# Performance work log

Hardware: AMD Instinct MI355X
Metric: run time of the kernel (lower is better)

The kernel has to match this reference:

```python
import jax, jax.numpy as jnp
import numpy as np

B, L, D_MODEL = 2, 2048, 1024
N_HEADS, D_K = 16, 64  # d_v == d_k (required by the output*q epilogue)


def setup_inputs() -> dict:
    key = jax.random.key(0)
    ks = jax.random.split(key, 8)
    # xavier_normal std for [d_model, d_k] fan: sqrt(2/(d_model+d_k))
    std = float(np.sqrt(2.0 / (D_MODEL + D_K)))
    std_p = float(np.sqrt(1.0 / (N_HEADS * D_K)))  # nn.Linear default ~ U(-1/sqrt(fan_in),..); normal approx ok for a baseline
    return {
        "q": jax.random.normal(ks[0], (B, L, D_MODEL), jnp.float32),
        "k": jax.random.normal(ks[1], (B, L, D_MODEL), jnp.float32),
        "v": jax.random.normal(ks[2], (B, L, D_MODEL), jnp.float32),
        "w_qs": jax.random.normal(ks[3], (N_HEADS, D_MODEL, D_K), jnp.float32) * std,
        "w_ks": jax.random.normal(ks[4], (N_HEADS, D_MODEL, D_K), jnp.float32) * std,
        "w_vs": jax.random.normal(ks[5], (N_HEADS, D_MODEL, D_K), jnp.float32) * std,
        "w_proj": jax.random.normal(ks[6], (D_MODEL, N_HEADS * D_K), jnp.float32) * std_p,
        "b_proj": jnp.zeros((D_MODEL,), jnp.float32),
    }


def reference(q, k, v, w_qs, w_ks, w_vs, w_proj, b_proj):
    # Per-head projections: [h, B, L, d_k]
    qh = jnp.einsum("bld,hdk->hblk", q, w_qs)
    kh = jnp.einsum("bld,hdk->hblk", k, w_ks)
    vh = jnp.einsum("bld,hdk->hblk", v, w_vs)
    # UNscaled attention (no 1/sqrt(d_k)), dropout is identity at eval
    attn = jax.nn.softmax(jnp.einsum("hblk,hbmk->hblm", qh, kh), axis=-1)
    # attn @ V with elementwise *q epilogue
    out = jnp.einsum("hblm,hbmk->hblk", attn, vh) * qh
    # torch.cat(torch.split(outputs, mb_size, 0), -1): heads concat on last dim
    out = out.transpose(1, 2, 0, 3).reshape(q.shape[0], q.shape[1], -1)  # [B, L, h*d_k]
    return out @ w_proj.T + b_proj
```

## Files before the change

kernel.cpp:

```cpp
#include <hip/hip_runtime.h>

#define B_ 2
#define L_ 2048
#define DM 1024
#define H_ 16
#define DK 64
#define ROWS (B_*L_)
#define BK 32
#define LDT 40

typedef _Float16 f16x8 __attribute__((ext_vector_type(8)));
typedef float    f32x4 __attribute__((ext_vector_type(4)));
typedef unsigned short us8 __attribute__((ext_vector_type(8)));
typedef unsigned short us4v __attribute__((ext_vector_type(4)));

__device__ __forceinline__ unsigned short f2h(float f) {
    _Float16 h = (_Float16)f;
    return __builtin_bit_cast(unsigned short, h);
}
__device__ __forceinline__ float h2f(unsigned short u) {
    return (float)__builtin_bit_cast(_Float16, u);
}
__device__ __forceinline__ f16x8 ld8h(const unsigned short* p) {
    return *reinterpret_cast<const f16x8*>(p);
}
__device__ __forceinline__ us8 cvt_us8(float4 a, float4 b) {
    us8 u;
    u[0] = f2h(a.x); u[1] = f2h(a.y); u[2] = f2h(a.z); u[3] = f2h(a.w);
    u[4] = f2h(b.x); u[5] = f2h(b.y); u[6] = f2h(b.z); u[7] = f2h(b.w);
    return u;
}

#define MFMA(a, b, c) __builtin_amdgcn_mfma_f32_16x16x32_f16((a), (b), (c), 0, 0, 0)

__global__ __launch_bounds__(256) void kcvt(
    const float* __restrict__ src, unsigned short* __restrict__ dst)
{
    size_t i = ((size_t)blockIdx.x * 256 + threadIdx.x) * 8;
    const float4* s4 = (const float4*)(src + i);
    *(us8*)(dst + i) = cvt_us8(s4[0], s4[1]);
}

__global__ __launch_bounds__(256) void k0_transpose_w(
    const float* __restrict__ wq,
    const float* __restrict__ wk,
    const float* __restrict__ wv,
    unsigned short* __restrict__ wt)
{
    __shared__ unsigned short tile[64][65];
    int bx = blockIdx.x;
    int which = bx / (H_ * 16);
    int rem   = bx % (H_ * 16);
    int h  = rem >> 4;
    int db = (rem & 15) * 64;
    const float* src = (which == 0) ? wq : (which == 1) ? wk : wv;

    int t = threadIdx.x;
    int r = t >> 2;
    int c = (t & 3) * 16;
    const float4* sp = (const float4*)(src + ((size_t)(h * DM + db + r)) * DK + c);
    #pragma unroll
    for (int i4 = 0; i4 < 4; i4++) {
        float4 f = sp[i4];
        tile[r][c + i4 * 4 + 0] = f2h(f.x);
        tile[r][c + i4 * 4 + 1] = f2h(f.y);
        tile[r][c + i4 * 4 + 2] = f2h(f.z);
        tile[r][c + i4 * 4 + 3] = f2h(f.w);
    }
    __syncthreads();

    int n   = t >> 2;
    int d16 = (t & 3) * 16;
    __align__(16) unsigned short ov[16];
    #pragma unroll
    for (int i = 0; i < 16; i++) ov[i] = tile[d16 + i][n];
    size_t off = (((size_t)which * H_ + h) * DK + n) * DM + db + d16;
    *(us8*)(wt + off)     = *(us8*)&ov[0];
    *(us8*)(wt + off + 8) = *(us8*)&ov[8];
}

__global__ __launch_bounds__(256) void k1_proj_qkv(
    const float* __restrict__ q,
    const float* __restrict__ k,
    const float* __restrict__ v,
    const unsigned short* __restrict__ wt,
    unsigned short* __restrict__ qh,
    unsigned short* __restrict__ kh,
    unsigned short* __restrict__ vt)
{
    __shared__ __align__(16) unsigned short sA[128 * LDT];
    __shared__ __align__(16) unsigned short sB[128 * LDT];

    int bx = blockIdx.x;
    int which = bx >> 8;
    int rem   = bx & 255;
    int mbase = (rem >> 3) * 128;
    int nbase = (rem & 7) * 128;

    const float* Ag = (which == 0) ? q : (which == 1) ? k : v;
    const unsigned short* Bg = wt + (size_t)which * DM * DM;

    int t = threadIdx.x;
    int wave = t >> 6, lane = t & 63, quad = lane >> 4, l16 = lane & 15;
    int wm = (wave >> 1) * 64, wn = (wave & 1) * 64;

    int ar0 = t >> 2,         ac0 = t & 3;
    int ar1 = (256 + t) >> 2, ac1 = t & 3;
    const float* pA0 = Ag + (size_t)(mbase + ar0) * DM + ac0 * 8;
    const float* pA1 = Ag + (size_t)(mbase + ar1) * DM + ac1 * 8;
    const unsigned short* pB0 = Bg + (size_t)(nbase + ar0) * DM + ac0 * 8;
    const unsigned short* pB1 = Bg + (size_t)(nbase + ar1) * DM + ac1 * 8;
    unsigned short* wA0 = &sA[ar0 * LDT + ac0 * 8];
    unsigned short* wA1 = &sA[ar1 * LDT + ac1 * 8];
    unsigned short* wB0 = &sB[ar0 * LDT + ac0 * 8];
    unsigned short* wB1 = &sB[ar1 * LDT + ac1 * 8];

    f32x4 acc[4][4];
    #pragma unroll
    for (int mi = 0; mi < 4; mi++)
        #pragma unroll
        for (int ni = 0; ni < 4; ni++) acc[mi][ni] = (f32x4)0.0f;

    float4 rA0a = *(const float4*)pA0, rA0b = *(const float4*)(pA0 + 4);
    float4 rA1a = *(const float4*)pA1, rA1b = *(const float4*)(pA1 + 4);
    us8 rB0 = *(const us8*)pB0, rB1 = *(const us8*)pB1;

    for (int step = 0; step < 32; step++) {
        if (step) __syncthreads();
        *(us8*)wA0 = cvt_us8(rA0a, rA0b);
        *(us8*)wA1 = cvt_us8(rA1a, rA1b);
        *(us8*)wB0 = rB0; *(us8*)wB1 = rB1;
        __syncthreads();
        if (step < 31) {
            pA0 += BK; pA1 += BK; pB0 += BK; pB1 += BK;
            rA0a = *(const float4*)pA0; rA0b = *(const float4*)(pA0 + 4);
            rA1a = *(const float4*)pA1; rA1b = *(const float4*)(pA1 + 4);
            rB0 = *(const us8*)pB0; rB1 = *(const us8*)pB1;
        }
        f16x8 aF[4], bF[4];
        #pragma unroll
        for (int mi = 0; mi < 4; mi++)
            aF[mi] = *(const f16x8*)&sA[(wm + mi * 16 + l16) * LDT + quad * 8];
        #pragma unroll
        for (int ni = 0; ni < 4; ni++)
            bF[ni] = *(const f16x8*)&sB[(wn + ni * 16 + l16) * LDT + quad * 8];
        #pragma unroll
        for (int mi = 0; mi < 4; mi++)
            #pragma unroll
            for (int ni = 0; ni < 4; ni++)
                acc[mi][ni] = MFMA(aF[mi], bF[ni], acc[mi][ni]);
    }

    int h = (nbase >> 6) + (wave & 1);
    if (which < 2) {
        unsigned short* OUT = ((which == 0) ? qh : kh) + (size_t)h * ROWS * DK;
        #pragma unroll
        for (int mi = 0; mi < 4; mi++)
            #pragma unroll
            for (int ni = 0; ni < 4; ni++)
                #pragma unroll
                for (int r = 0; r < 4; r++) {
                    int row = mbase + wm + mi * 16 + quad * 4 + r;
                    OUT[(size_t)row * DK + ni * 16 + l16] = f2h(acc[mi][ni][r]);
                }
    } else {
        unsigned short* OUT = vt + (size_t)h * DK * ROWS;
        #pragma unroll
        for (int mi = 0; mi < 4; mi++)
            #pragma unroll
            for (int ni = 0; ni < 4; ni++) {
                int dk   = ni * 16 + l16;
                int rowb = mbase + wm + mi * 16 + quad * 4;
                us4v pk;
                pk[0] = f2h(acc[mi][ni][0]); pk[1] = f2h(acc[mi][ni][1]);
                pk[2] = f2h(acc[mi][ni][2]); pk[3] = f2h(acc[mi][ni][3]);
                *(us4v*)(OUT + (size_t)dk * ROWS + rowb) = pk;
            }
    }
}

__global__ __launch_bounds__(256) void k2_attn(
    const unsigned short* __restrict__ qh,
    const unsigned short* __restrict__ kh,
    const unsigned short* __restrict__ vt,
    unsigned short* __restrict__ x2)
{
    __shared__ __align__(16) unsigned short ktile[64][72];
    __shared__ __align__(16) unsigned short vtile[64][72];
    __shared__ __align__(16) unsigned short pld[4][16][72];

    int bx = blockIdx.x;
    int xcd = bx & 7;
    int loc = bx >> 3;
    int hb  = xcd * 4 + (loc >> 5);
    int qt  = loc & 31;
    int h = hb >> 1, b = hb & 1;
    int qbase = qt * 64;

    const unsigned short* qhp = qh + ((size_t)h * ROWS + b * L_) * DK;
    const unsigned short* khp = kh + ((size_t)h * ROWS + b * L_) * DK;
    const unsigned short* vtp = vt + (size_t)h * DK * ROWS + b * L_;

    int wave = threadIdx.x >> 6, lane = threadIdx.x & 63;
    int quad = lane >> 4, l16 = lane & 15;
    int t = threadIdx.x;

    int qrow = qbase + wave * 16 + l16;
    f16x8 qb0 = ld8h(qhp + (size_t)qrow * DK + quad * 8);
    f16x8 qb1 = ld8h(qhp + (size_t)qrow * DK + 32 + quad * 8);

    float m_i = -1e30f, l_i = 0.0f;
    f32x4 o[4];
    #pragma unroll
    for (int nt = 0; nt < 4; nt++) o[nt] = (f32x4)0.0f;

    for (int kt = 0; kt < 32; kt++) {
        int kb = kt * 64;
        {
            const unsigned short* kg = khp + (size_t)kb * DK;
            #pragma unroll
            for (int i = 0; i < 2; i++) {
                int c = i * 256 + t;
                int key = c >> 3, ch = (c & 7) * 8;
                *(us8*)&ktile[key][ch] = *(const us8*)(kg + c * 8);
            }
            #pragma unroll
            for (int i = 0; i < 2; i++) {
                int c = i * 256 + t;
                int dk = c >> 3, ch = (c & 7) * 8;
                *(us8*)&vtile[dk][ch] = *(const us8*)(vtp + (size_t)dk * ROWS + kb + ch);
            }
        }
        __syncthreads();

        f32x4 s[4];
        #pragma unroll
        for (int nt = 0; nt < 4; nt++) s[nt] = (f32x4)0.0f;
        #pragma unroll
        for (int nt = 0; nt < 4; nt++) {
            f16x8 ka0 = *(const f16x8*)&ktile[nt * 16 + l16][quad * 8];
            f16x8 ka1 = *(const f16x8*)&ktile[nt * 16 + l16][32 + quad * 8];
            s[nt] = MFMA(ka0, qb0, s[nt]);
            s[nt] = MFMA(ka1, qb1, s[nt]);
        }

        float mx = s[0][0];
        #pragma unroll
        for (int nt = 0; nt < 4; nt++)
            #pragma unroll
            for (int r = 0; r < 4; r++) mx = fmaxf(mx, s[nt][r]);
        mx = fmaxf(mx, __shfl_xor(mx, 16));
        mx = fmaxf(mx, __shfl_xor(mx, 32));
        float mnew  = fmaxf(m_i, mx);
        float alpha = __expf(m_i - mnew);
        float rs = 0.0f;
        #pragma unroll
        for (int nt = 0; nt < 4; nt++)
            #pragma unroll
            for (int r = 0; r < 4; r++) {
                float pv = __expf(s[nt][r] - mnew);
                s[nt][r] = pv;
                rs += pv;
            }
        rs += __shfl_xor(rs, 16);
        rs += __shfl_xor(rs, 32);
        l_i = l_i * alpha + rs;
        m_i = mnew;

        #pragma unroll
        for (int r = 0; r < 4; r++) {
            float av = __shfl(alpha, quad * 4 + r);
            #pragma unroll
            for (int nt = 0; nt < 4; nt++) o[nt][r] *= av;
        }

        #pragma unroll
        for (int nt = 0; nt < 4; nt++) {
            us4v pk;
            pk[0] = f2h(s[nt][0]); pk[1] = f2h(s[nt][1]);
            pk[2] = f2h(s[nt][2]); pk[3] = f2h(s[nt][3]);
            *(us4v*)&pld[wave][l16][nt * 16 + quad * 4] = pk;
        }

        #pragma unroll
        for (int kk = 0; kk < 2; kk++) {
            f16x8 pa = *(const f16x8*)&pld[wave][l16][kk * 32 + quad * 8];
            #pragma unroll
            for (int nt = 0; nt < 4; nt++) {
                f16x8 vb = *(const f16x8*)&vtile[nt * 16 + l16][kk * 32 + quad * 8];
                o[nt] = MFMA(pa, vb, o[nt]);
            }
        }
        __syncthreads();
    }

    float linv = 1.0f / l_i;
    #pragma unroll
    for (int r = 0; r < 4; r++) {
        float lv = __shfl(linv, quad * 4 + r);
        int row = qbase + wave * 16 + quad * 4 + r;
        #pragma unroll
        for (int nt = 0; nt < 4; nt++) {
            int col = nt * 16 + l16;
            float qv = h2f(qhp[(size_t)row * DK + col]);
            float val = o[nt][r] * lv * qv;
            x2[((size_t)b * L_ + row) * DM + h * DK + col] = f2h(val);
        }
    }
}

__global__ __launch_bounds__(256) void k3_out_proj(
    const unsigned short* __restrict__ x2,
    const unsigned short* __restrict__ wph,
    const float* __restrict__ bias,
    float* __restrict__ out)
{
    __shared__ __align__(16) unsigned short sA[128 * LDT];
    __shared__ __align__(16) unsigned short sB[128 * LDT];

    int bx = blockIdx.x;
    int mbase = (bx >> 3) * 128;
    int nbase = (bx & 7) * 128;

    int t = threadIdx.x;
    int wave = t >> 6, lane = t & 63, quad = lane >> 4, l16 = lane & 15;
    int wm = (wave >> 1) * 64, wn = (wave & 1) * 64;

    int ar0 = t >> 2,         ac0 = t & 3;
    int ar1 = (256 + t) >> 2, ac1 = t & 3;
    const unsigned short* pA0 = x2 + (size_t)(mbase + ar0) * DM + ac0 * 8;
    const unsigned short* pA1 = x2 + (size_t)(mbase + ar1) * DM + ac1 * 8;
    const unsigned short* pB0 = wph + (size_t)(nbase + ar0) * DM + ac0 * 8;
    const unsigned short* pB1 = wph + (size_t)(nbase + ar1) * DM + ac1 * 8;
    unsigned short* wA0 = &sA[ar0 * LDT + ac0 * 8];
    unsigned short* wA1 = &sA[ar1 * LDT + ac1 * 8];
    unsigned short* wB0 = &sB[ar0 * LDT + ac0 * 8];
    unsigned short* wB1 = &sB[ar1 * LDT + ac1 * 8];

    f32x4 acc[4][4];
    #pragma unroll
    for (int mi = 0; mi < 4; mi++)
        #pragma unroll
        for (int ni = 0; ni < 4; ni++) acc[mi][ni] = (f32x4)0.0f;

    us8 rA0 = *(const us8*)pA0, rA1 = *(const us8*)pA1;
    us8 rB0 = *(const us8*)pB0, rB1 = *(const us8*)pB1;

    for (int step = 0; step < 32; step++) {
        if (step) __syncthreads();
        *(us8*)wA0 = rA0; *(us8*)wA1 = rA1;
        *(us8*)wB0 = rB0; *(us8*)wB1 = rB1;
        __syncthreads();
        if (step < 31) {
            pA0 += BK; pA1 += BK; pB0 += BK; pB1 += BK;
            rA0 = *(const us8*)pA0; rA1 = *(const us8*)pA1;
            rB0 = *(const us8*)pB0; rB1 = *(const us8*)pB1;
        }
        f16x8 aF[4], bF[4];
        #pragma unroll
        for (int mi = 0; mi < 4; mi++)
            aF[mi] = *(const f16x8*)&sA[(wm + mi * 16 + l16) * LDT + quad * 8];
        #pragma unroll
        for (int ni = 0; ni < 4; ni++)
            bF[ni] = *(const f16x8*)&sB[(wn + ni * 16 + l16) * LDT + quad * 8];
        #pragma unroll
        for (int mi = 0; mi < 4; mi++)
            #pragma unroll
            for (int ni = 0; ni < 4; ni++)
                acc[mi][ni] = MFMA(aF[mi], bF[ni], acc[mi][ni]);
    }

    float bv[4];
    #pragma unroll
    for (int ni = 0; ni < 4; ni++) bv[ni] = bias[nbase + wn + ni * 16 + l16];

    #pragma unroll
    for (int mi = 0; mi < 4; mi++)
        #pragma unroll
        for (int ni = 0; ni < 4; ni++)
            #pragma unroll
            for (int r = 0; r < 4; r++) {
                int row = mbase + wm + mi * 16 + quad * 4 + r;
                int col = nbase + wn + ni * 16 + l16;
                out[(size_t)row * DM + col] = acc[mi][ni][r] + bv[ni];
            }
}

extern "C" void kernel_launch(void* const* d_in, const int* in_sizes, int n_in,
                              void* d_out, int out_size, void* d_ws, size_t ws_size,
                              hipStream_t stream)
{
    const float* q     = (const float*)d_in[0];
    const float* k     = (const float*)d_in[1];
    const float* v     = (const float*)d_in[2];
    const float* wqs   = (const float*)d_in[3];
    const float* wks   = (const float*)d_in[4];
    const float* wvs   = (const float*)d_in[5];
    const float* wproj = (const float*)d_in[6];
    const float* bproj = (const float*)d_in[7];
    float* out = (float*)d_out;

    char* ws = (char*)d_ws;
    #define MB (size_t)(1024 * 1024)
    unsigned short* wt  = (unsigned short*)(ws);
    unsigned short* wph = (unsigned short*)(ws + 6  * MB);
    unsigned short* qh  = (unsigned short*)(ws + 8  * MB);
    unsigned short* kh  = (unsigned short*)(ws + 16 * MB);
    unsigned short* vt  = (unsigned short*)(ws + 24 * MB);
    unsigned short* x2  = (unsigned short*)(ws + 32 * MB);

    kcvt<<<dim3((DM * DM) / (256 * 8)), dim3(256), 0, stream>>>(wproj, wph);
    k0_transpose_w<<<dim3(3 * H_ * 16), dim3(256), 0, stream>>>(wqs, wks, wvs, wt);

    k1_proj_qkv<<<dim3(3 * 32 * 8), dim3(256), 0, stream>>>(q, k, v, wt, qh, kh, vt);
    k2_attn<<<dim3(H_ * B_ * 32), dim3(256), 0, stream>>>(qh, kh, vt, x2);
    k3_out_proj<<<dim3(32 * 8), dim3(256), 0, stream>>>(x2, wph, bproj, out);
}
```

Baseline: 263.1 us.

## Double-buffer K tiles, load V directly into registers, lazily rescale softmax

The attention kernel now double-buffers the K tile in shared memory. The next tile is prefetched into registers during compute, so each iteration needs only one barrier instead of two. V fragments are read straight from global memory into registers, skipping the shared-memory V tile. The online softmax only rescales the running max and accumulators when the new row max grows by more than 8, which saves exp and multiply work. The trade-offs are more register pressure, uncoalesced direct global V loads, and a bounded growth of exponent values under the lazy rescale.

```diff
diff --git a/kernel.cpp b/kernel.cpp
--- a/kernel.cpp
+++ b/kernel.cpp
@@ -185,8 +185,7 @@
     const unsigned short* __restrict__ vt,
     unsigned short* __restrict__ x2)
 {
-    __shared__ __align__(16) unsigned short ktile[64][72];
-    __shared__ __align__(16) unsigned short vtile[64][72];
+    __shared__ __align__(16) unsigned short ktile[2][64][72];
     __shared__ __align__(16) unsigned short pld[4][16][72];
 
     int bx = blockIdx.x;
@@ -205,6 +204,9 @@
     int quad = lane >> 4, l16 = lane & 15;
     int t = threadIdx.x;
 
+    int key0 = t >> 3,         kch0 = (t & 7) * 8;
+    int key1 = (256 + t) >> 3, kch1 = (t & 7) * 8;
+
     int qrow = qbase + wave * 16 + l16;
     f16x8 qb0 = ld8h(qhp + (size_t)qrow * DK + quad * 8);
     f16x8 qb1 = ld8h(qhp + (size_t)qrow * DK + 32 + quad * 8);
@@ -214,35 +216,39 @@
     #pragma unroll
     for (int nt = 0; nt < 4; nt++) o[nt] = (f32x4)0.0f;
 
+    us8 kr0 = *(const us8*)(khp + (size_t)t * 8);
+    us8 kr1 = *(const us8*)(khp + (size_t)(256 + t) * 8);
+    *(us8*)&ktile[0][key0][kch0] = kr0;
+    *(us8*)&ktile[0][key1][kch1] = kr1;
+    __syncthreads();
+
+    int cur = 0;
     for (int kt = 0; kt < 32; kt++) {
         int kb = kt * 64;
-        {
-            const unsigned short* kg = khp + (size_t)kb * DK;
-            #pragma unroll
-            for (int i = 0; i < 2; i++) {
-                int c = i * 256 + t;
-                int key = c >> 3, ch = (c & 7) * 8;
-                *(us8*)&ktile[key][ch] = *(const us8*)(kg + c * 8);
-            }
-            #pragma unroll
-            for (int i = 0; i < 2; i++) {
-                int c = i * 256 + t;
-                int dk = c >> 3, ch = (c & 7) * 8;
-                *(us8*)&vtile[dk][ch] = *(const us8*)(vtp + (size_t)dk * ROWS + kb + ch);
-            }
-        }
-        __syncthreads();
 
         f32x4 s[4];
         #pragma unroll
         for (int nt = 0; nt < 4; nt++) s[nt] = (f32x4)0.0f;
         #pragma unroll
         for (int nt = 0; nt < 4; nt++) {
-            f16x8 ka0 = *(const f16x8*)&ktile[nt * 16 + l16][quad * 8];
-            f16x8 ka1 = *(const f16x8*)&ktile[nt * 16 + l16][32 + quad * 8];
+            f16x8 ka0 = *(const f16x8*)&ktile[cur][nt * 16 + l16][quad * 8];
+            f16x8 ka1 = *(const f16x8*)&ktile[cur][nt * 16 + l16][32 + quad * 8];
             s[nt] = MFMA(ka0, qb0, s[nt]);
             s[nt] = MFMA(ka1, qb1, s[nt]);
         }
+
+        if (kt < 31) {
+            const unsigned short* kg = khp + (size_t)(kb + 64) * DK;
+            kr0 = *(const us8*)(kg + (size_t)t * 8);
+            kr1 = *(const us8*)(kg + (size_t)(256 + t) * 8);
+        }
+        f16x8 vbr[2][4];
+        #pragma unroll
+        for (int kk = 0; kk < 2; kk++)
+            #pragma unroll
+            for (int nt = 0; nt < 4; nt++)
+                vbr[kk][nt] = ld8h(vtp + (size_t)(nt * 16 + l16) * ROWS
+                                       + kb + kk * 32 + quad * 8);
 
         float mx = s[0][0];
         #pragma unroll
@@ -251,28 +257,32 @@
             for (int r = 0; r < 4; r++) mx = fmaxf(mx, s[nt][r]);
         mx = fmaxf(mx, __shfl_xor(mx, 16));
         mx = fmaxf(mx, __shfl_xor(mx, 32));
-        float mnew  = fmaxf(m_i, mx);
-        float alpha = __expf(m_i - mnew);
+
+        if (!__all(mx - m_i <= 8.0f)) {
+            float mnew  = fmaxf(m_i, mx);
+            float alpha = __expf(m_i - mnew);
+            l_i *= alpha;
+            #pragma unroll
+            for (int r = 0; r < 4; r++) {
+                float av = __shfl(alpha, quad * 4 + r);
+                #pragma unroll
+                for (int nt = 0; nt < 4; nt++) o[nt][r] *= av;
+            }
+            m_i = mnew;
+        }
+
         float rs = 0.0f;
         #pragma unroll
         for (int nt = 0; nt < 4; nt++)
             #pragma unroll
             for (int r = 0; r < 4; r++) {
-                float pv = __expf(s[nt][r] - mnew);
+                float pv = __expf(s[nt][r] - m_i);
                 s[nt][r] = pv;
                 rs += pv;
             }
         rs += __shfl_xor(rs, 16);
         rs += __shfl_xor(rs, 32);
-        l_i = l_i * alpha + rs;
-        m_i = mnew;
-
-        #pragma unroll
-        for (int r = 0; r < 4; r++) {
-            float av = __shfl(alpha, quad * 4 + r);
-            #pragma unroll
-            for (int nt = 0; nt < 4; nt++) o[nt][r] *= av;
-        }
+        l_i += rs;
 
         #pragma unroll
         for (int nt = 0; nt < 4; nt++) {
@@ -286,12 +296,16 @@
         for (int kk = 0; kk < 2; kk++) {
             f16x8 pa = *(const f16x8*)&pld[wave][l16][kk * 32 + quad * 8];
             #pragma unroll
-            for (int nt = 0; nt < 4; nt++) {
-                f16x8 vb = *(const f16x8*)&vtile[nt * 16 + l16][kk * 32 + quad * 8];
-                o[nt] = MFMA(pa, vb, o[nt]);
-            }
+            for (int nt = 0; nt < 4; nt++)
+                o[nt] = MFMA(pa, vbr[kk][nt], o[nt]);
+        }
+
+        if (kt < 31) {
+            *(us8*)&ktile[cur ^ 1][key0][kch0] = kr0;
+            *(us8*)&ktile[cur ^ 1][key1][kch1] = kr1;
         }
         __syncthreads();
+        cur ^= 1;
     }
 
     float linv = 1.0f / l_i;
```

Result: slower. 338.2 us (+28.5%).

## Use base-2 softmax with log2e folded into K weights and lazy rescaling

Applied to the files above, without the earlier changes.

Multiplies the K projection weights by log2(e) during weight conversion, so attention scores come out in the base-2 domain and the softmax can call the hardware exp2 directly. The running max and the rescaling of the output accumulator are now skipped unless some lane's max grows by more than 11, which saves exps, shuffles and multiplies in most iterations. The max and sum reductions become trees, and s_setprio raises wave priority around the MFMA blocks. In exchange, unnormalized probabilities can reach 2^11, which narrows the fp16 headroom for P, and K is rounded to fp16 after scaling.

```diff
diff --git a/kernel.cpp b/kernel.cpp
--- a/kernel.cpp
+++ b/kernel.cpp
@@ -54,6 +54,7 @@
     int h  = rem >> 4;
     int db = (rem & 15) * 64;
     const float* src = (which == 0) ? wq : (which == 1) ? wk : wv;
+    float scale = (which == 1) ? 1.44269504f : 1.0f;
 
     int t = threadIdx.x;
     int r = t >> 2;
@@ -62,10 +63,10 @@
     #pragma unroll
     for (int i4 = 0; i4 < 4; i4++) {
         float4 f = sp[i4];
-        tile[r][c + i4 * 4 + 0] = f2h(f.x);
-        tile[r][c + i4 * 4 + 1] = f2h(f.y);
-        tile[r][c + i4 * 4 + 2] = f2h(f.z);
-        tile[r][c + i4 * 4 + 3] = f2h(f.w);
+        tile[r][c + i4 * 4 + 0] = f2h(f.x * scale);
+        tile[r][c + i4 * 4 + 1] = f2h(f.y * scale);
+        tile[r][c + i4 * 4 + 2] = f2h(f.z * scale);
+        tile[r][c + i4 * 4 + 3] = f2h(f.w * scale);
     }
     __syncthreads();
 
@@ -236,6 +237,7 @@
         f32x4 s[4];
         #pragma unroll
         for (int nt = 0; nt < 4; nt++) s[nt] = (f32x4)0.0f;
+        __builtin_amdgcn_s_setprio(1);
         #pragma unroll
         for (int nt = 0; nt < 4; nt++) {
             f16x8 ka0 = *(const f16x8*)&ktile[nt * 16 + l16][quad * 8];
@@ -243,36 +245,46 @@
             s[nt] = MFMA(ka0, qb0, s[nt]);
             s[nt] = MFMA(ka1, qb1, s[nt]);
         }
-
-        float mx = s[0][0];
-        #pragma unroll
-        for (int nt = 0; nt < 4; nt++)
-            #pragma unroll
-            for (int r = 0; r < 4; r++) mx = fmaxf(mx, s[nt][r]);
+        __builtin_amdgcn_s_setprio(0);
+
+        float pm[4];
+        #pragma unroll
+        for (int nt = 0; nt < 4; nt++) {
+            float a = fmaxf(s[nt][0], s[nt][1]);
+            float c2 = fmaxf(s[nt][2], s[nt][3]);
+            pm[nt] = fmaxf(a, c2);
+        }
+        float mx = fmaxf(fmaxf(pm[0], pm[1]), fmaxf(pm[2], pm[3]));
         mx = fmaxf(mx, __shfl_xor(mx, 16));
         mx = fmaxf(mx, __shfl_xor(mx, 32));
-        float mnew  = fmaxf(m_i, mx);
-        float alpha = __expf(m_i - mnew);
-        float rs = 0.0f;
-        #pragma unroll
-        for (int nt = 0; nt < 4; nt++)
+
+        if (!__all(mx - m_i <= 11.0f)) {
+            float mnew  = fmaxf(m_i, mx);
+            float alpha = __builtin_amdgcn_exp2f(m_i - mnew);
+            l_i *= alpha;
             #pragma unroll
             for (int r = 0; r < 4; r++) {
-                float pv = __expf(s[nt][r] - mnew);
-                s[nt][r] = pv;
-                rs += pv;
-            }
+                float av = __shfl(alpha, quad * 4 + r);
+                #pragma unroll
+                for (int nt = 0; nt < 4; nt++) o[nt][r] *= av;
+            }
+            m_i = mnew;
+        }
+
+        float ps[4];
+        #pragma unroll
+        for (int nt = 0; nt < 4; nt++) {
+            float e0 = __builtin_amdgcn_exp2f(s[nt][0] - m_i);
+            float e1 = __builtin_amdgcn_exp2f(s[nt][1] - m_i);
+            float e2 = __builtin_amdgcn_exp2f(s[nt][2] - m_i);
+            float e3 = __builtin_amdgcn_exp2f(s[nt][3] - m_i);
+            s[nt][0] = e0; s[nt][1] = e1; s[nt][2] = e2; s[nt][3] = e3;
+            ps[nt] = (e0 + e1) + (e2 + e3);
+        }
+        float rs = (ps[0] + ps[1]) + (ps[2] + ps[3]);
         rs += __shfl_xor(rs, 16);
         rs += __shfl_xor(rs, 32);
-        l_i = l_i * alpha + rs;
-        m_i = mnew;
-
-        #pragma unroll
-        for (int r = 0; r < 4; r++) {
-            float av = __shfl(alpha, quad * 4 + r);
-            #pragma unroll
-            for (int nt = 0; nt < 4; nt++) o[nt][r] *= av;
-        }
+        l_i += rs;
 
         #pragma unroll
         for (int nt = 0; nt < 4; nt++) {
@@ -282,6 +294,7 @@
             *(us4v*)&pld[wave][l16][nt * 16 + quad * 4] = pk;
         }
 
+        __builtin_amdgcn_s_setprio(1);
         #pragma unroll
         for (int kk = 0; kk < 2; kk++) {
             f16x8 pa = *(const f16x8*)&pld[wave][l16][kk * 32 + quad * 8];
@@ -291,6 +304,7 @@
                 o[nt] = MFMA(pa, vb, o[nt]);
             }
         }
+        __builtin_amdgcn_s_setprio(0);
         __syncthreads();
     }
 
```

New measurement: 260.7 us. Within noise of the previous version (-0.9%).
